# Kernel optimization log

Hardware: AMD Instinct MI355X
Metric: run time of the kernel (lower is better)

## Reference

```python
import jax, jax.numpy as jnp
import numpy as np

N_NODES = 8192
D = 7      # in_dim == out_dim (hardcoded 7x7 weight)
K = 32     # kNN fan-out


def setup_inputs() -> dict:
    key = jax.random.key(0)
    k1, k2, k3 = jax.random.split(key, 3)
    x = jax.random.normal(k1, (N_NODES, D + 1), dtype=jnp.float32)
    W = jax.random.normal(k2, (D, D), dtype=jnp.float32) * np.float32(1.0 / np.sqrt(D))
    a = jax.random.normal(k3, (2 * D,), dtype=jnp.float32) * np.float32(0.1)
    return {"x": x, "W": W, "a": a}


def _forward(x, W, a, k=K):
    # split pollutant channel (last column) from features, as in the torch forward
    pollutant = x[:, -1]          # (N,)
    feat = x[:, :-1]              # (N, D)
    N, d = feat.shape

    # linear transform (nn.functional.linear(x, weight) == x @ W.T)
    out = feat @ W.T              # (N, D)
    # nonlinearity_1 = Hardtanh
    out = jnp.clip(out, -1.0, 1.0)
    # (feature_weight = softmax(a) is computed in torch but unused for 'affine' kernel)

    # kNN graph built from input features (use_previous_graph=True).
    # Squared distances give the same neighbor ordering as euclidean norms.
    sq = jnp.sum(feat * feat, axis=1)                       # (N,)
    dist2 = sq[:, None] + sq[None, :] - 2.0 * (feat @ feat.T)
    dist2 = jnp.maximum(dist2, 0.0)
    dist2 = jnp.where(jnp.eye(N, dtype=bool), jnp.inf, dist2)  # dist[dist==0] = inf (self)
    _, nbr = jax.lax.top_k(-dist2, k)                       # (N, k) nearest neighbors

    out_n = out[nbr]                                        # (N, k, D) neighbor gather
    # affine attention: score_ij = concat(out_i, out_j) . a
    s = (out @ a[:d])[:, None] + out_n @ a[d:]              # (N, k)
    att = jax.nn.softmax(s, axis=-1)                        # per-node softmax over neighbors

    pol_n = pollutant[nbr]                                  # (N, k)
    xp = jnp.concatenate([out_n, pol_n[..., None]], axis=-1)  # (N, k, D+1)
    agg = jnp.einsum('nk,nkd->nd', att, xp)                 # attention-weighted aggregate

    y = jnp.concatenate([out, agg], axis=-1)                # (N, 2D+1)
    return y, att


def reference(x, W, a):
    y, att = _forward(x, W, a)
    # torch returns (y, y_, a) where y_ is y and a is the last node's attention row
    return (y, y, att[-1])
```

## Files before the change

kernel.cpp:

```cpp
#include <hip/hip_runtime.h>
#include <math.h>
#include <stdint.h>

#define N_NODES 8192
#define D 7
#define K 32
#define NT 512
#define QB 8
#define CPT (N_NODES / NT)
#define ECAP 384
#define ECAP2 256
#define DELTA 0.25f

typedef unsigned long long u64;
typedef _Float16 h2 __attribute__((ext_vector_type(2)));

__device__ __forceinline__ float rfl(float v) {
    return __uint_as_float(__builtin_amdgcn_readfirstlane(__float_as_uint(v)));
}
__device__ __forceinline__ unsigned rflu(unsigned v) {
    return __builtin_amdgcn_readfirstlane(v);
}
__device__ __forceinline__ h2 h2u(unsigned u) {
    union { unsigned u; h2 h; } t; t.u = u; return t.h;
}
__device__ __forceinline__ unsigned pkh(float a, float b) {
    union { h2 h; unsigned u; } t;
    t.h[0] = (_Float16)a; t.h[1] = (_Float16)b; return t.u;
}
__device__ __forceinline__ unsigned ordu(float f) {
    unsigned u = __float_as_uint(f);
    return (u & 0x80000000u) ? ~u : (u | 0x80000000u);
}
__device__ __forceinline__ float unordu(unsigned o) {
    unsigned u = (o & 0x80000000u) ? (o & 0x7fffffffu) : ~o;
    return __uint_as_float(u);
}

#if __has_builtin(__builtin_amdgcn_fdot2)
#define FDOT2(a, b, c) __builtin_amdgcn_fdot2((a), (b), (c), false)
#else
__device__ __forceinline__ float FDOT2(h2 a, h2 b, float c) {
    return fmaf((float)a[1], (float)b[1], fmaf((float)a[0], (float)b[0], c));
}
#endif

__device__ __forceinline__ float dist_m(float4 b0, float4 b1, float sqj,
                                        float4 A, float4 B) {
    float dot = A.x * b0.x;
    dot = fmaf(A.y, b0.y, dot);
    dot = fmaf(A.z, b0.z, dot);
    dot = fmaf(A.w, b0.w, dot);
    dot = fmaf(B.x, b1.x, dot);
    dot = fmaf(B.y, b1.y, dot);
    dot = fmaf(B.z, b1.z, dot);
    return fmaf(-2.0f, dot, sqj);
}

__device__ __forceinline__ float screen_m(uint4 dj, unsigned s0, unsigned s1,
                                          unsigned s2, unsigned s3) {
    return FDOT2(h2u(dj.x), h2u(s0),
           FDOT2(h2u(dj.y), h2u(s1),
           FDOT2(h2u(dj.z), h2u(s2),
           FDOT2(h2u(dj.w), h2u(s3), 0.f))));
}

__global__ __launch_bounds__(256)
void precompute_kernel(const float* __restrict__ x, const float* __restrict__ W,
                       float* __restrict__ outb, float* __restrict__ sqb,
                       uint4* __restrict__ fh)
{
    int n = blockIdx.x * 256 + threadIdx.x;
    float4 v0 = *reinterpret_cast<const float4*>(x + n * 8);
    float4 v1 = *reinterpret_cast<const float4*>(x + n * 8 + 4);
    float f[D] = {v0.x, v0.y, v0.z, v0.w, v1.x, v1.y, v1.z};
    float sq = 0.f;
#pragma unroll
    for (int c = 0; c < D; ++c) sq += f[c] * f[c];
    sqb[n] = sq;
    uint4 h;
    h.x = pkh(f[0], f[1]); h.y = pkh(f[2], f[3]);
    h.z = pkh(f[4], f[5]); h.w = pkh(f[6], sq);
    fh[n] = h;
#pragma unroll
    for (int r = 0; r < D; ++r) {
        float acc = 0.f;
#pragma unroll
        for (int c = 0; c < D; ++c) acc += f[c] * W[r * D + c];
        acc = fminf(fmaxf(acc, -1.f), 1.f);
        outb[n * D + r] = acc;
    }
}

__global__ __launch_bounds__(NT, 4)
void gat_kernel(const float* __restrict__ x, const float* __restrict__ aw,
                const float* __restrict__ outb, const float* __restrict__ sqb,
                const uint4* __restrict__ fh, float* __restrict__ dout)
{
    __shared__ u64      cand[QB][ECAP2];
    __shared__ unsigned short ent[QB][ECAP];
    __shared__ int      nbr[QB][K];
    __shared__ unsigned selT[QB];
    __shared__ float    exthL[QB];
    __shared__ int      scnt[QB];
    __shared__ int      cnt2[QB];
    __shared__ float    qf[QB][8];
    __shared__ float    redv[8];
    __shared__ int      redi[8];
    __shared__ float    bcv;
    __shared__ int      bci;

    float* Lmin = (float*)cand;

    const int tid  = threadIdx.x;
    const int lane = tid & 63;
    const int wave = tid >> 6;
    const int i0   = blockIdx.x * QB;

    unsigned qs0[QB], qs1[QB], qs2[QB], qs3[QB];
    float sqi[QB];
#pragma unroll
    for (int q = 0; q < QB; ++q) {
        const float* xq = x + (i0 + q) * 8;
        float4 a0 = *reinterpret_cast<const float4*>(xq);
        float4 a1 = *reinterpret_cast<const float4*>(xq + 4);
        qs0[q] = rflu(pkh(-2.f * a0.x, -2.f * a0.y));
        qs1[q] = rflu(pkh(-2.f * a0.z, -2.f * a0.w));
        qs2[q] = rflu(pkh(-2.f * a1.x, -2.f * a1.y));
        qs3[q] = rflu(pkh(-2.f * a1.z, 1.0f));
        sqi[q] = rfl(sqb[i0 + q]);
    }
    if (tid < QB) {
        const float* xq = x + (i0 + tid) * 8;
#pragma unroll
        for (int c = 0; c < D; ++c) qf[tid][c] = xq[c];
        qf[tid][7] = sqb[i0 + tid];
        scnt[tid] = 0;
        cnt2[tid] = 0;
    }

    float lm[QB];
#pragma unroll
    for (int q = 0; q < QB; ++q) lm[q] = INFINITY;

#pragma unroll 4
    for (int c = 0; c < CPT; ++c) {
        uint4 dj = fh[c * NT + tid];
#pragma unroll
        for (int q = 0; q < QB; ++q)
            lm[q] = fminf(lm[q], screen_m(dj, qs0[q], qs1[q], qs2[q], qs3[q]));
    }

#pragma unroll
    for (int q = 0; q < QB; ++q) Lmin[q * NT + tid] = lm[q];
    __syncthreads();

    {
        const int q = wave;
        unsigned ov0 = ordu(Lmin[q * NT +   0 + lane]);
        unsigned ov1 = ordu(Lmin[q * NT +  64 + lane]);
        unsigned ov2 = ordu(Lmin[q * NT + 128 + lane]);
        unsigned ov3 = ordu(Lmin[q * NT + 192 + lane]);
        unsigned ov4 = ordu(Lmin[q * NT + 256 + lane]);
        unsigned ov5 = ordu(Lmin[q * NT + 320 + lane]);
        unsigned ov6 = ordu(Lmin[q * NT + 384 + lane]);
        unsigned ov7 = ordu(Lmin[q * NT + 448 + lane]);
        unsigned lo = 0u, hi = 0xFFFFFFFFu;
        while (lo < hi) {
            unsigned mid = lo + ((hi - lo) >> 1);
            int cnt = __popcll(__ballot(ov0 <= mid))
                    + __popcll(__ballot(ov1 <= mid))
                    + __popcll(__ballot(ov2 <= mid))
                    + __popcll(__ballot(ov3 <= mid))
                    + __popcll(__ballot(ov4 <= mid))
                    + __popcll(__ballot(ov5 <= mid))
                    + __popcll(__ballot(ov6 <= mid))
                    + __popcll(__ballot(ov7 <= mid));
            if (cnt >= 33) hi = mid; else lo = mid + 1;
        }
        if (lane == 0) selT[q] = lo;
    }
    __syncthreads();

    float kthr[QB];
#pragma unroll
    for (int q = 0; q < QB; ++q) {
        float Ts = unordu(selT[q]);
        kthr[q] = fmaxf(Ts + 2.f * DELTA, -sqi[q] + DELTA);
    }
    if (tid < QB) {
        float Ts = unordu(selT[tid]);
        exthL[tid] = fmaxf(Ts + DELTA, -qf[tid][7]);
    }

#pragma unroll 4
    for (int c = 0; c < CPT; ++c) {
        int j = c * NT + tid;
        uint4 dj = fh[j];
#pragma unroll
        for (int q = 0; q < QB; ++q) {
            float m = screen_m(dj, qs0[q], qs1[q], qs2[q], qs3[q]);
            if (m <= kthr[q] && j != i0 + q) {
                int p = atomicAdd(&scnt[q], 1);
                if (p < ECAP) ent[q][p] = (unsigned short)j;
            }
        }
    }
    __syncthreads();

    const float4* xb = reinterpret_cast<const float4*>(x);
#pragma unroll 1
    for (int q = 0; q < QB; ++q) {
        int n = scnt[q];
        if (n > ECAP) n = ECAP;
        float4 A  = *reinterpret_cast<const float4*>(&qf[q][0]);
        float4 Bv = *reinterpret_cast<const float4*>(&qf[q][4]);
        float thr = exthL[q];
        for (int t = tid; t < n; t += NT) {
            int j = ent[q][t];
            float4 b0 = xb[j * 2];
            float4 b1 = xb[j * 2 + 1];
            float m   = dist_m(b0, b1, sqb[j], A, Bv);
            if (m <= thr) {
                float d2c = fmaxf(Bv.w + m, 0.f);
                u64 key = ((u64)__float_as_uint(d2c) << 32) | (unsigned)j;
                int p = atomicAdd(&cnt2[q], 1);
                if (p < ECAP2) cand[q][p] = key;
            }
        }
    }
    __syncthreads();

    {
        const int q = wave;
        const int M = cnt2[q];
        if (scnt[q] <= ECAP && M >= K && M <= ECAP2) {
            for (int p = lane; p < M; p += 64) {
                u64 my = cand[q][p];
                int rank = 0;
                for (int m = 0; m < M; ++m)
                    rank += (cand[q][m] < my) ? 1 : 0;
                if (rank < K) nbr[q][rank] = (int)(my & 0xffffffffu);
            }
        }
    }
    __syncthreads();

#pragma unroll 1
    for (int q = 0; q < QB; ++q) {
        int s = scnt[q];
        int M = cnt2[q];
        if (s > ECAP || M < K || M > ECAP2) {
            const int iq = i0 + q;
            const float* xq = x + iq * 8;
            float4 A  = *reinterpret_cast<const float4*>(xq);
            float4 Bv = *reinterpret_cast<const float4*>(xq + 4);
            Bv.w = sqb[iq];
            float lastv = -1.0f; int lasti = -1;
#pragma unroll 1
            for (int it = 0; it < K; ++it) {
                float best = INFINITY; int bidx = 0x7fffffff;
#pragma unroll 1
                for (int c = 0; c < CPT; ++c) {
                    int j = c * NT + tid;
                    float4 b0 = xb[j * 2];
                    float4 b1 = xb[j * 2 + 1];
                    float m = dist_m(b0, b1, sqb[j], A, Bv);
                    float d2c = fmaxf(Bv.w + m, 0.f);
                    if (j == iq) continue;
                    bool gt = (d2c > lastv) || (d2c == lastv && j > lasti);
                    if (gt && (d2c < best || (d2c == best && j < bidx))) {
                        best = d2c; bidx = j;
                    }
                }
#pragma unroll
                for (int off = 32; off > 0; off >>= 1) {
                    float ov = __shfl_down(best, off);
                    int   oi = __shfl_down(bidx, off);
                    if (ov < best || (ov == best && oi < bidx)) { best = ov; bidx = oi; }
                }
                if (lane == 0) { redv[wave] = best; redi[wave] = bidx; }
                __syncthreads();
                if (tid == 0) {
                    float bv = redv[0]; int bi = redi[0];
#pragma unroll
                    for (int w = 1; w < 8; ++w)
                        if (redv[w] < bv || (redv[w] == bv && redi[w] < bi)) {
                            bv = redv[w]; bi = redi[w];
                        }
                    bcv = bv; bci = bi;
                    nbr[q][it] = bi;
                }
                __syncthreads();
                lastv = bcv; lasti = bci;
            }
        }
    }
    __syncthreads();

    {
        const int q  = wave;
        const int iq = i0 + q;
        if (lane < K) {
            int nk = nbr[q][lane];
            float s = 0.f;
#pragma unroll
            for (int c = 0; c < D; ++c) s += outb[iq * D + c] * aw[c];
            float xp[D + 1];
#pragma unroll
            for (int c = 0; c < D; ++c) {
                float on = outb[nk * D + c];
                xp[c] = on;
                s += on * aw[D + c];
            }
            xp[D] = x[nk * 8 + 7];

            float m = s;
#pragma unroll
            for (int off = 16; off > 0; off >>= 1) m = fmaxf(m, __shfl_xor(m, off, 32));
            float e = expf(s - m);
            float sum = e;
#pragma unroll
            for (int off = 16; off > 0; off >>= 1) sum += __shfl_xor(sum, off, 32);
            float att = e / sum;

            float agg[D + 1];
#pragma unroll
            for (int dd = 0; dd < D + 1; ++dd) {
                float v = att * xp[dd];
#pragma unroll
                for (int off = 16; off > 0; off >>= 1) v += __shfl_xor(v, off, 32);
                agg[dd] = v;
            }

            if (lane < D) {
                float o = outb[iq * D + lane];
                dout[iq * 15 + lane] = o;
                dout[N_NODES * 15 + iq * 15 + lane] = o;
            }
            if (lane < D + 1) {
                float av_ = agg[0];
#pragma unroll
                for (int dd = 1; dd < D + 1; ++dd) av_ = (lane == dd) ? agg[dd] : av_;
                dout[iq * 15 + D + lane] = av_;
                dout[N_NODES * 15 + iq * 15 + D + lane] = av_;
            }
            if (iq == N_NODES - 1) dout[2 * N_NODES * 15 + lane] = att;
        }
    }
}

extern "C" void kernel_launch(void* const* d_in, const int* in_sizes, int n_in,
                              void* d_out, int out_size, void* d_ws, size_t ws_size,
                              hipStream_t stream) {
    (void)in_sizes; (void)n_in; (void)out_size; (void)ws_size;
    const float* x = (const float*)d_in[0];
    const float* W = (const float*)d_in[1];
    const float* a = (const float*)d_in[2];
    float* out  = (float*)d_out;
    float* outb = (float*)d_ws;
    float* sqb  = outb + N_NODES * D;
    uint4* fh   = (uint4*)(sqb + N_NODES);

    hipLaunchKernelGGL(precompute_kernel, dim3(N_NODES / 256), dim3(256),
                       0, stream, x, W, outb, sqb, fh);
    hipLaunchKernelGGL(gat_kernel, dim3(N_NODES / QB), dim3(NT),
                       0, stream, x, a, outb, sqb, fh, out);
}
```

Before: 71.38 us.

## Estimate kNN threshold from a subsample and filter candidates in exact fp32 in one pass

The threshold-estimation pass now scans only the first SUBC chunks of nodes instead of all of them. It picks the 34th-smallest per-lane minimum as the threshold estimate. The fp16 screen plus separate exact-refinement pass is replaced by one fp32 distance pass over all nodes, reading a packed float4 layout with the squared norm folded in, with a tighter DELTA. This removes a full fp16 scan and the entry-list stage. The cost is fp32 math over every node, and a looser subsample threshold may push more queries into the slow fallback path.

```diff
diff --git a/kernel.cpp b/kernel.cpp
--- a/kernel.cpp
+++ b/kernel.cpp
@@ -8,9 +8,9 @@
 #define NT 512
 #define QB 8
 #define CPT (N_NODES / NT)
-#define ECAP 384
+#define SUBC 8
 #define ECAP2 256
-#define DELTA 0.25f
+#define DELTA 0.125f
 
 typedef unsigned long long u64;
 typedef _Float16 h2 __attribute__((ext_vector_type(2)));
@@ -67,8 +67,8 @@
 
 __global__ __launch_bounds__(256)
 void precompute_kernel(const float* __restrict__ x, const float* __restrict__ W,
-                       float* __restrict__ outb, float* __restrict__ sqb,
-                       uint4* __restrict__ fh)
+                       float* __restrict__ outb, uint4* __restrict__ fh,
+                       float4* __restrict__ xsq4)
 {
     int n = blockIdx.x * 256 + threadIdx.x;
     float4 v0 = *reinterpret_cast<const float4*>(x + n * 8);
@@ -77,11 +77,12 @@
     float sq = 0.f;
 #pragma unroll
     for (int c = 0; c < D; ++c) sq += f[c] * f[c];
-    sqb[n] = sq;
     uint4 h;
     h.x = pkh(f[0], f[1]); h.y = pkh(f[2], f[3]);
     h.z = pkh(f[4], f[5]); h.w = pkh(f[6], sq);
     fh[n] = h;
+    xsq4[n * 2]     = v0;
+    xsq4[n * 2 + 1] = make_float4(v1.x, v1.y, v1.z, sq);
 #pragma unroll
     for (int r = 0; r < D; ++r) {
         float acc = 0.f;
@@ -94,17 +95,13 @@
 
 __global__ __launch_bounds__(NT, 4)
 void gat_kernel(const float* __restrict__ x, const float* __restrict__ aw,
-                const float* __restrict__ outb, const float* __restrict__ sqb,
-                const uint4* __restrict__ fh, float* __restrict__ dout)
+                const float* __restrict__ outb, const uint4* __restrict__ fh,
+                const float4* __restrict__ xs4, float* __restrict__ dout)
 {
     __shared__ u64      cand[QB][ECAP2];
-    __shared__ unsigned short ent[QB][ECAP];
     __shared__ int      nbr[QB][K];
     __shared__ unsigned selT[QB];
-    __shared__ float    exthL[QB];
-    __shared__ int      scnt[QB];
     __shared__ int      cnt2[QB];
-    __shared__ float    qf[QB][8];
     __shared__ float    redv[8];
     __shared__ int      redi[8];
     __shared__ float    bcv;
@@ -118,39 +115,37 @@
     const int i0   = blockIdx.x * QB;
 
     unsigned qs0[QB], qs1[QB], qs2[QB], qs3[QB];
+    float4 qA[QB], qBv[QB];
     float sqi[QB];
 #pragma unroll
     for (int q = 0; q < QB; ++q) {
         const float* xq = x + (i0 + q) * 8;
         float4 a0 = *reinterpret_cast<const float4*>(xq);
         float4 a1 = *reinterpret_cast<const float4*>(xq + 4);
+        float sq_ = rfl(xs4[(i0 + q) * 2 + 1].w);
         qs0[q] = rflu(pkh(-2.f * a0.x, -2.f * a0.y));
         qs1[q] = rflu(pkh(-2.f * a0.z, -2.f * a0.w));
         qs2[q] = rflu(pkh(-2.f * a1.x, -2.f * a1.y));
         qs3[q] = rflu(pkh(-2.f * a1.z, 1.0f));
-        sqi[q] = rfl(sqb[i0 + q]);
-    }
-    if (tid < QB) {
-        const float* xq = x + (i0 + tid) * 8;
-#pragma unroll
-        for (int c = 0; c < D; ++c) qf[tid][c] = xq[c];
-        qf[tid][7] = sqb[i0 + tid];
-        scnt[tid] = 0;
-        cnt2[tid] = 0;
-    }
+        qA[q].x  = rfl(a0.x); qA[q].y  = rfl(a0.y);
+        qA[q].z  = rfl(a0.z); qA[q].w  = rfl(a0.w);
+        qBv[q].x = rfl(a1.x); qBv[q].y = rfl(a1.y);
+        qBv[q].z = rfl(a1.z); qBv[q].w = sq_;
+        sqi[q]   = sq_;
+    }
+    if (tid < QB) cnt2[tid] = 0;
 
     float lm[QB];
 #pragma unroll
     for (int q = 0; q < QB; ++q) lm[q] = INFINITY;
 
 #pragma unroll 4
-    for (int c = 0; c < CPT; ++c) {
+    for (int c = 0; c < SUBC; ++c) {
         uint4 dj = fh[c * NT + tid];
 #pragma unroll
         for (int q = 0; q < QB; ++q)
             lm[q] = fminf(lm[q], screen_m(dj, qs0[q], qs1[q], qs2[q], qs3[q]));
     }
-
 #pragma unroll
     for (int q = 0; q < QB; ++q) Lmin[q * NT + tid] = lm[q];
     __syncthreads();
@@ -176,53 +171,27 @@
                     + __popcll(__ballot(ov5 <= mid))
                     + __popcll(__ballot(ov6 <= mid))
                     + __popcll(__ballot(ov7 <= mid));
-            if (cnt >= 33) hi = mid; else lo = mid + 1;
+            if (cnt >= 34) hi = mid; else lo = mid + 1;
         }
         if (lane == 0) selT[q] = lo;
     }
     __syncthreads();
 
-    float kthr[QB];
-#pragma unroll
-    for (int q = 0; q < QB; ++q) {
-        float Ts = unordu(selT[q]);
-        kthr[q] = fmaxf(Ts + 2.f * DELTA, -sqi[q] + DELTA);
-    }
-    if (tid < QB) {
-        float Ts = unordu(selT[tid]);
-        exthL[tid] = fmaxf(Ts + DELTA, -qf[tid][7]);
-    }
-
-#pragma unroll 4
+    float exq[QB];
+#pragma unroll
+    for (int q = 0; q < QB; ++q)
+        exq[q] = fmaxf(unordu(selT[q]) + DELTA, -sqi[q]);
+
+#pragma unroll 2
     for (int c = 0; c < CPT; ++c) {
         int j = c * NT + tid;
-        uint4 dj = fh[j];
+        float4 b0 = xs4[j * 2];
+        float4 b1 = xs4[j * 2 + 1];
 #pragma unroll
         for (int q = 0; q < QB; ++q) {
-            float m = screen_m(dj, qs0[q], qs1[q], qs2[q], qs3[q]);
-            if (m <= kthr[q] && j != i0 + q) {
-                int p = atomicAdd(&scnt[q], 1);
-                if (p < ECAP) ent[q][p] = (unsigned short)j;
-            }
-        }
-    }
-    __syncthreads();
-
-    const float4* xb = reinterpret_cast<const float4*>(x);
-#pragma unroll 1
-    for (int q = 0; q < QB; ++q) {
-        int n = scnt[q];
-        if (n > ECAP) n = ECAP;
-        float4 A  = *reinterpret_cast<const float4*>(&qf[q][0]);
-        float4 Bv = *reinterpret_cast<const float4*>(&qf[q][4]);
-        float thr = exthL[q];
-        for (int t = tid; t < n; t += NT) {
-            int j = ent[q][t];
-            float4 b0 = xb[j * 2];
-            float4 b1 = xb[j * 2 + 1];
-            float m   = dist_m(b0, b1, sqb[j], A, Bv);
-            if (m <= thr) {
-                float d2c = fmaxf(Bv.w + m, 0.f);
+            float m = dist_m(b0, b1, b1.w, qA[q], qBv[q]);
+            if (m <= exq[q] && j != i0 + q) {
+                float d2c = fmaxf(sqi[q] + m, 0.f);
                 u64 key = ((u64)__float_as_uint(d2c) << 32) | (unsigned)j;
                 int p = atomicAdd(&cnt2[q], 1);
                 if (p < ECAP2) cand[q][p] = key;
@@ -234,7 +203,7 @@
     {
         const int q = wave;
         const int M = cnt2[q];
-        if (scnt[q] <= ECAP && M >= K && M <= ECAP2) {
+        if (M >= K && M <= ECAP2) {
             for (int p = lane; p < M; p += 64) {
                 u64 my = cand[q][p];
                 int rank = 0;
@@ -248,14 +217,13 @@
 
 #pragma unroll 1
     for (int q = 0; q < QB; ++q) {
-        int s = scnt[q];
         int M = cnt2[q];
-        if (s > ECAP || M < K || M > ECAP2) {
+        if (M < K || M > ECAP2) {
             const int iq = i0 + q;
             const float* xq = x + iq * 8;
             float4 A  = *reinterpret_cast<const float4*>(xq);
             float4 Bv = *reinterpret_cast<const float4*>(xq + 4);
-            Bv.w = sqb[iq];
+            Bv.w = xs4[iq * 2 + 1].w;
             float lastv = -1.0f; int lasti = -1;
 #pragma unroll 1
             for (int it = 0; it < K; ++it) {
@@ -263,9 +231,9 @@
 #pragma unroll 1
                 for (int c = 0; c < CPT; ++c) {
                     int j = c * NT + tid;
-                    float4 b0 = xb[j * 2];
-                    float4 b1 = xb[j * 2 + 1];
-                    float m = dist_m(b0, b1, sqb[j], A, Bv);
+                    float4 b0 = xs4[j * 2];
+                    float4 b1 = xs4[j * 2 + 1];
+                    float m = dist_m(b0, b1, b1.w, A, Bv);
                     float d2c = fmaxf(Bv.w + m, 0.f);
                     if (j == iq) continue;
                     bool gt = (d2c > lastv) || (d2c == lastv && j > lasti);
@@ -357,13 +325,13 @@
     const float* x = (const float*)d_in[0];
     const float* W = (const float*)d_in[1];
     const float* a = (const float*)d_in[2];
-    float* out  = (float*)d_out;
-    float* outb = (float*)d_ws;
-    float* sqb  = outb + N_NODES * D;
-    uint4* fh   = (uint4*)(sqb + N_NODES);
+    float* out   = (float*)d_out;
+    float* outb  = (float*)d_ws;
+    uint4* fh    = (uint4*)(outb + N_NODES * D);
+    float4* xsq4 = (float4*)(fh + N_NODES);
 
     hipLaunchKernelGGL(precompute_kernel, dim3(N_NODES / 256), dim3(256),
-                       0, stream, x, W, outb, sqb, fh);
+                       0, stream, x, W, outb, fh, xsq4);
     hipLaunchKernelGGL(gat_kernel, dim3(N_NODES / QB), dim3(NT),
-                       0, stream, x, a, outb, sqb, fh, out);
-}
+                       0, stream, x, a, outb, fh, xsq4, out);
+}
```

Result: slower. 73.11 us (+2.4%).
